# Kernel optimization log

Measured on AMD Instinct MI355X. Metric: run time of the kernel, lower is better.

Reference implementation:

```python
import jax, jax.numpy as jnp
import numpy as np

B = 131072
DIM = 64
D_IN = 32
D_OUT = 32
HIDDEN = 512
N_BINS = 8
TAIL = 3.0


def setup_inputs() -> dict:
    key = jax.random.key(0)
    ks = jax.random.split(key, 7)
    x = jax.random.normal(ks[0], (B, DIM), dtype=jnp.float32)
    out_dim = D_OUT * (3 * N_BINS - 1)  # 32 * 23 = 736
    W1 = jax.random.normal(ks[1], (D_IN, HIDDEN), dtype=jnp.float32) / np.sqrt(D_IN)
    b1 = jnp.zeros((HIDDEN,), dtype=jnp.float32)
    W2 = jax.random.normal(ks[2], (HIDDEN, HIDDEN), dtype=jnp.float32) / np.sqrt(HIDDEN)
    b2 = jnp.zeros((HIDDEN,), dtype=jnp.float32)
    W3 = jax.random.normal(ks[3], (HIDDEN, out_dim), dtype=jnp.float32) / np.sqrt(HIDDEN)
    b3 = jnp.zeros((out_dim,), dtype=jnp.float32)
    return {"x": x, "W1": W1, "b1": b1, "W2": W2, "b2": b2, "W3": W3, "b3": b3}


def _gather(t, idx):
    # t: (..., K), idx: (...) -> (...,)
    return jnp.take_along_axis(t, idx[..., None], axis=-1)[..., 0]


def rq_spline_forward(x, widths, heights, derivatives, tail_bound=TAIL):
    K = widths.shape[-1]
    widths = jax.nn.softmax(widths, axis=-1) * 2 * tail_bound
    heights = jax.nn.softmax(heights, axis=-1) * 2 * tail_bound
    derivatives = jax.nn.softplus(derivatives)
    ones = jnp.ones_like(derivatives[..., :1])
    derivatives = jnp.concatenate([ones, derivatives, ones], axis=-1)  # (..., K+1)
    cumwidths = jnp.cumsum(widths, axis=-1)
    cumwidths = jnp.pad(cumwidths, [(0, 0)] * (cumwidths.ndim - 1) + [(1, 0)]) - tail_bound
    cumheights = jnp.cumsum(heights, axis=-1)
    cumheights = jnp.pad(cumheights, [(0, 0)] * (cumheights.ndim - 1) + [(1, 0)]) - tail_bound

    inside = (x >= -tail_bound) & (x <= tail_bound)
    xc = jnp.clip(x, -tail_bound + 1e-6, tail_bound - 1e-6)
    # searchsorted (left): number of knots strictly less than xc
    bin_idx = jnp.sum(cumwidths[..., 1:] < xc[..., None], axis=-1)
    bin_idx = jnp.clip(bin_idx, 0, K - 1)

    w_k = _gather(widths, bin_idx)
    h_k = _gather(heights, bin_idx)
    d_k = _gather(derivatives, bin_idx)
    d_k1 = _gather(derivatives[..., 1:], bin_idx)
    cw_k = _gather(cumwidths, bin_idx)
    ch_k = _gather(cumheights, bin_idx)

    xi = jnp.clip((xc - cw_k) / w_k, 1e-6, 1 - 1e-6)
    s_k = h_k / w_k
    num = h_k * (s_k * xi**2 + d_k * xi * (1 - xi))
    den = s_k + (d_k + d_k1 - 2 * s_k) * xi * (1 - xi)
    y_inside = ch_k + num / den
    log_det_inside = (
        jnp.log(s_k**2 * (d_k1 * xi**2 + 2 * s_k * xi * (1 - xi) + d_k * (1 - xi) ** 2) + 1e-8)
        - jnp.log(den**2 + 1e-8)
    )
    y = jnp.where(inside, y_inside, x)
    log_det = jnp.where(inside, log_det_inside, jnp.zeros_like(x))
    return y, log_det


def reference(x, W1, b1, W2, b2, W3, b3):
    # mask: first D_IN dims conditioned on, last D_OUT transformed
    x_masked = x[:, :D_IN]
    x_transform = x[:, D_IN:]
    h = jax.nn.relu(x_masked @ W1 + b1)
    h = jax.nn.relu(h @ W2 + b2)
    raw = h @ W3 + b3
    raw = raw.reshape(x.shape[0], D_OUT, 3 * N_BINS - 1)
    widths = raw[..., :N_BINS]
    heights = raw[..., N_BINS:2 * N_BINS]
    derivs = raw[..., 2 * N_BINS:]
    y_t, log_det = rq_spline_forward(x_transform, widths, heights, derivs, TAIL)
    y = jnp.concatenate([x_masked, y_t], axis=-1)
    return y, jnp.sum(log_det, axis=-1)
```

## Files before the change

### kernel.cpp

```cpp
#include <hip/hip_runtime.h>
#include <hip/hip_bf16.h>
#include <stdint.h>

typedef __bf16 bf16_t;
typedef _Float16 f16_t;
typedef _Float16 f16x8 __attribute__((ext_vector_type(8)));
typedef _Float16 f16x4 __attribute__((ext_vector_type(4)));
typedef float f32x4 __attribute__((ext_vector_type(4)));

#define HID 512
#define NRAW 736
#define NRAW_PAD 768
#define TAILB 3.0f

__device__ __forceinline__ void glds16(const void* g, void* s) {
  __builtin_amdgcn_global_load_lds(
      (const __attribute__((address_space(1))) void*)g,
      (__attribute__((address_space(3))) void*)s, 16, 0, 0);
}
__device__ __forceinline__ float frcp(float x) { return __builtin_amdgcn_rcpf(x); }

__global__ void detect_dtype(const void* x, int* flag) {
  __shared__ int s;
  if (threadIdx.x == 0) s = 0;
  __syncthreads();
  const bf16_t* xb = (const bf16_t*)x;
  int cnt = 0;
  for (int j = 0; j < 16; j++) {
    float v = (float)xb[threadIdx.x * 16 + j];
    if (!(v == v) || fabsf(v) > 64.0f) cnt++;
  }
  atomicAdd(&s, cnt);
  __syncthreads();
  if (threadIdx.x == 0) *flag = (s > 64) ? 1 : 0;
}

__global__ void conv_wb(const void* W1, const void* W2, const void* W3,
                        const void* b1, const void* b2, const void* b3,
                        f16_t* __restrict__ w1t, f16_t* __restrict__ w2t,
                        f16_t* __restrict__ w3t,
                        float* __restrict__ bf1, float* __restrict__ bf2,
                        float* __restrict__ bf3, const int* flagp) {
  const int flag = *flagp;
  auto rd = [&](const void* p, size_t idx) -> float {
    return flag ? ((const float*)p)[idx] : (float)((const bf16_t*)p)[idx];
  };
  int i = blockIdx.x * 256 + threadIdx.x;
  if (i < 512 * 32)  { w1t[i] = (f16_t)rd(W1, (size_t)(i & 31) * 512 + (i >> 5)); return; }
  i -= 512 * 32;
  if (i < 512 * 512) { w2t[i] = (f16_t)rd(W2, (size_t)(i & 511) * 512 + (i >> 9)); return; }
  i -= 512 * 512;
  if (i < NRAW_PAD * 512) {
    int n = i >> 9, k = i & 511;
    int ch = n / 24, e = n % 24;
    w3t[i] = (e < 23) ? (f16_t)rd(W3, (size_t)k * NRAW + ch * 23 + e) : (f16_t)0.0f;
    return;
  }
  i -= NRAW_PAD * 512;
  if (i < 512) { bf1[i] = rd(b1, i); return; }
  i -= 512;
  if (i < 512) { bf2[i] = rd(b2, i); return; }
  i -= 512;
  if (i < NRAW_PAD) {
    int ch = i / 24, e = i % 24;
    bf3[i] = (e < 23) ? rd(b3, (size_t)ch * 23 + e) : 0.0f;
  }
}

__global__ void convert_x(const void* x, void* __restrict__ outv,
                          const int* flagp, int n) {
  const int flag = *flagp;
  const int i0 = (blockIdx.x * 256 + threadIdx.x) * 8;
  if (i0 >= n) return;
  const int row = i0 >> 5, col = i0 & 31;
  const size_t src = (size_t)row * 64 + col;
  if (flag) {
    const float4* s4 = (const float4*)((const float*)x + src);
    float4* d4 = (float4*)((float*)outv + src);
    d4[0] = s4[0]; d4[1] = s4[1];
  } else {
    *(uint4*)((bf16_t*)outv + src) = *(const uint4*)((const bf16_t*)x + src);
  }
}

__global__ void ld_finalize(const float* __restrict__ ldp, void* __restrict__ outv,
                            const int* __restrict__ flagp, int M) {
  const int i = blockIdx.x * 256 + threadIdx.x;
  if (i >= M) return;
  float s = 0.f;
  #pragma unroll
  for (int n = 0; n < 4; n++) s += ldp[(size_t)n * M + i];
  if (*flagp) ((float*)outv)[(size_t)M * 64 + i] = s;
  else        ((bf16_t*)outv)[(size_t)M * 64 + i] = (bf16_t)s;
}

__launch_bounds__(256)
__global__ void gemm12(const void* __restrict__ xorig, const f16_t* __restrict__ W1t,
                       const float* __restrict__ b1, const f16_t* __restrict__ W2t,
                       const float* __restrict__ b2, f16_t* __restrict__ H2,
                       int r0, const int* __restrict__ flagp) {
  constexpr int BK = 64;
  constexpr int BUF = 128 * BK;
  __shared__ __align__(16) f16_t As[2 * BUF], Bs[2 * BUF];
  const int t = threadIdx.x;
  const int id = blockIdx.x;
  const int xcd = id & 7, s = id >> 3;
  const int n0 = (s & 3) * 128;
  const int m0 = ((s >> 2) * 8 + xcd) * 128;
  const int lrow = t >> 3, lcb = t & 7;
  const int lane = t & 63, w = t >> 6;
  const int wr = (w >> 1) * 64, wc = (w & 1) * 64, wc2 = (w & 1) * 32;
  const int lm = lane & 15, quad = lane >> 4;
  const int flag = *flagp;

  const f16_t* gb[4];
  f16_t* ldb[4];
  #pragma unroll
  for (int r = 0; r < 4; r++) {
    const int row = r * 32 + lrow;
    const int gc = (lcb ^ (row & 7)) * 8;
    gb[r] = W2t + (size_t)(n0 + row) * 512 + gc;
    ldb[r] = &Bs[row * BK + lcb * 8];
  }
  int apo[4][2], bpo[4][2];
  #pragma unroll
  for (int i = 0; i < 4; i++) {
    const int ra = wr + i * 16 + lm, rb = wc + i * 16 + lm;
    #pragma unroll
    for (int ksi = 0; ksi < 2; ksi++) {
      const int qb = ksi * 4 + quad;
      apo[i][ksi] = ra * BK + ((qb ^ (ra & 7)) << 3);
      bpo[i][ksi] = rb * BK + ((qb ^ (rb & 7)) << 3);
    }
  }
  f16x8 xfr[4];
  #pragma unroll
  for (int i = 0; i < 4; i++) {
    const size_t xrow = (size_t)(r0 + m0 + wr + i * 16 + lm);
    if (flag) {
      const float* px = (const float*)xorig + xrow * 64 + quad * 8;
      const float4 a = *(const float4*)px;
      const float4 b = *(const float4*)(px + 4);
      f16x8 v;
      v[0] = (f16_t)a.x; v[1] = (f16_t)a.y; v[2] = (f16_t)a.z; v[3] = (f16_t)a.w;
      v[4] = (f16_t)b.x; v[5] = (f16_t)b.y; v[6] = (f16_t)b.z; v[7] = (f16_t)b.w;
      xfr[i] = v;
    } else {
      const bf16_t* px = (const bf16_t*)xorig + xrow * 64 + quad * 8;
      f16x8 v;
      #pragma unroll
      for (int j = 0; j < 8; j++) v[j] = (f16_t)(float)px[j];
      xfr[i] = v;
    }
  }
  const f16_t* w1p0 = W1t + (size_t)(wc2 + lm) * 32 + quad * 8;
  const f16_t* w1p1 = W1t + (size_t)(wc2 + 16 + lm) * 32 + quad * 8;
  const float* b1p0 = b1 + wc2 + 4 * quad;
  const float* b1p1 = b1 + wc2 + 16 + 4 * quad;
  int woff[4][2];
  #pragma unroll
  for (int i = 0; i < 4; i++) {
    const int row = wr + i * 16 + lm;
    #pragma unroll
    for (int Tl = 0; Tl < 2; Tl++) {
      const int cb = (wc2 >> 3) + 2 * Tl + (quad >> 1);
      woff[i][Tl] = row * BK + ((cb ^ (row & 7)) << 3) + 4 * (quad & 1);
    }
  }

  f32x4 acc[4][4] = {};

  {
    f16x8 w1f0 = *(const f16x8*)w1p0;
    f16x8 w1f1 = *(const f16x8*)w1p1;
    const float4 bv0 = *(const float4*)b1p0;
    const float4 bv1 = *(const float4*)b1p1;
    #pragma unroll
    for (int r = 0; r < 4; r++) glds16(gb[r], ldb[r]);
    #pragma unroll
    for (int i = 0; i < 4; i++) {
      f32x4 z = {};
      const f32x4 h0 = __builtin_amdgcn_mfma_f32_16x16x32_f16(w1f0, xfr[i], z, 0, 0, 0);
      const f32x4 h1 = __builtin_amdgcn_mfma_f32_16x16x32_f16(w1f1, xfr[i], z, 0, 0, 0);
      f16x4 v0, v1;
      v0[0] = (f16_t)fmaxf(h0[0] + bv0.x, 0.0f);
      v0[1] = (f16_t)fmaxf(h0[1] + bv0.y, 0.0f);
      v0[2] = (f16_t)fmaxf(h0[2] + bv0.z, 0.0f);
      v0[3] = (f16_t)fmaxf(h0[3] + bv0.w, 0.0f);
      v1[0] = (f16_t)fmaxf(h1[0] + bv1.x, 0.0f);
      v1[1] = (f16_t)fmaxf(h1[1] + bv1.y, 0.0f);
      v1[2] = (f16_t)fmaxf(h1[2] + bv1.z, 0.0f);
      v1[3] = (f16_t)fmaxf(h1[3] + bv1.w, 0.0f);
      *(f16x4*)&As[woff[i][0]] = v0;
      *(f16x4*)&As[woff[i][1]] = v1;
    }
  }
  f16x8 w1fa = *(const f16x8*)(w1p0 + (size_t)64 * 32);
  f16x8 w1fb = *(const f16x8*)(w1p1 + (size_t)64 * 32);
  float4 bva = *(const float4*)(b1p0 + 64);
  float4 bvb = *(const float4*)(b1p1 + 64);
  __syncthreads();

  #pragma unroll
  for (int k = 0; k < 8; k++) {
    const int cur = k & 1, nb = cur ^ 1;
    if (k < 7) {
      #pragma unroll
      for (int r = 0; r < 4; r++)
        glds16(gb[r] + (k + 1) * 64, ldb[r] + nb * BUF);
      #pragma unroll
      for (int i = 0; i < 4; i++) {
        f32x4 z = {};
        const f32x4 h0 = __builtin_amdgcn_mfma_f32_16x16x32_f16(w1fa, xfr[i], z, 0, 0, 0);
        const f32x4 h1 = __builtin_amdgcn_mfma_f32_16x16x32_f16(w1fb, xfr[i], z, 0, 0, 0);
        f16x4 v0, v1;
        v0[0] = (f16_t)fmaxf(h0[0] + bva.x, 0.0f);
        v0[1] = (f16_t)fmaxf(h0[1] + bva.y, 0.0f);
        v0[2] = (f16_t)fmaxf(h0[2] + bva.z, 0.0f);
        v0[3] = (f16_t)fmaxf(h0[3] + bva.w, 0.0f);
        v1[0] = (f16_t)fmaxf(h1[0] + bvb.x, 0.0f);
        v1[1] = (f16_t)fmaxf(h1[1] + bvb.y, 0.0f);
        v1[2] = (f16_t)fmaxf(h1[2] + bvb.z, 0.0f);
        v1[3] = (f16_t)fmaxf(h1[3] + bvb.w, 0.0f);
        *(f16x4*)&As[nb * BUF + woff[i][0]] = v0;
        *(f16x4*)&As[nb * BUF + woff[i][1]] = v1;
      }
      if (k < 6) {
        w1fa = *(const f16x8*)(w1p0 + (size_t)(k + 2) * 64 * 32);
        w1fb = *(const f16x8*)(w1p1 + (size_t)(k + 2) * 64 * 32);
        bva = *(const float4*)(b1p0 + (k + 2) * 64);
        bvb = *(const float4*)(b1p1 + (k + 2) * 64);
      }
    }
    #pragma unroll
    for (int ksi = 0; ksi < 2; ksi++) {
      f16x8 af[4], bf[4];
      #pragma unroll
      for (int i = 0; i < 4; i++) af[i] = *(const f16x8*)&As[cur * BUF + apo[i][ksi]];
      #pragma unroll
      for (int j = 0; j < 4; j++) bf[j] = *(const f16x8*)&Bs[cur * BUF + bpo[j][ksi]];
      __builtin_amdgcn_s_setprio(1);
      #pragma unroll
      for (int i = 0; i < 4; i++)
        #pragma unroll
        for (int j = 0; j < 4; j++)
          acc[i][j] = __builtin_amdgcn_mfma_f32_16x16x32_f16(af[i], bf[j], acc[i][j], 0, 0, 0);
      __builtin_amdgcn_s_setprio(0);
    }
    if (k < 7) __syncthreads();
  }
  #pragma unroll
  for (int i = 0; i < 4; i++)
    #pragma unroll
    for (int j = 0; j < 4; j++) {
      const int col = n0 + wc + j * 16 + lm;
      const float bv = b2[col];
      #pragma unroll
      for (int r = 0; r < 4; r++) {
        const int rowi = m0 + wr + i * 16 + quad * 4 + r;
        H2[(size_t)rowi * HID + col] = (f16_t)fmaxf(acc[i][j][r] + bv, 0.0f);
      }
    }
}

#define RSH 200
#define SP1 0.5413248546f

__launch_bounds__(512, 4)
__global__ void gemm3_spline(const f16_t* __restrict__ A, const f16_t* __restrict__ Bt,
                             const float* __restrict__ bias,
                             const void* __restrict__ xorig,
                             void* __restrict__ outv, float* __restrict__ ldp,
                             int M, int r0, const int* __restrict__ flagp) {
  __shared__ __align__(16) f16_t lds[2 * 8192 + 2 * 12288];
  f16_t* As = lds;
  f16_t* Bs = lds + 2 * 8192;
  f16_t* rawh = lds;

  const int t = threadIdx.x;
  const int id = blockIdx.x;
  const int xcd = id & 7, sloc = id >> 3;
  const int cpx = gridDim.x >> 3;
  const int wg = xcd * cpx + sloc;
  const int ntile = wg & 3;
  const int m0 = (wg >> 2) * 128;
  const int n0 = ntile * 192;
  const int lane = t & 63, w = t >> 6;
  const int lm = lane & 15, quad = lane >> 4;
  const int wrow = (w >> 2) * 64, wcol = (w & 3) * 48;
  const int lrow = t >> 3, lcb = t & 7;
  const int flag = *flagp;

  const int gc = (lcb ^ (lrow & 7)) * 8;
  const f16_t* gA = A + (size_t)(m0 + lrow) * 512 + gc;
  const f16_t* gB = Bt + (size_t)(n0 + lrow) * 512 + gc;
  f16_t* ldA = As + lrow * 64 + lcb * 8;
  f16_t* ldB = Bs + lrow * 64 + lcb * 8;

  int aoff[4], boff[3];
  #pragma unroll
  for (int i = 0; i < 4; i++) {
    const int ra = wrow + i * 16 + lm;
    aoff[i] = ra * 64 + ((quad ^ (ra & 7)) << 3);
  }
  #pragma unroll
  for (int j = 0; j < 3; j++) {
    const int rb = wcol + j * 16 + lm;
    boff[j] = rb * 64 + ((quad ^ (rb & 7)) << 3);
  }

  const int prow = t >> 3, pch = t & 7;
  float xt_pre[2];
  #pragma unroll
  for (int e = 0; e < 2; e++) {
    const size_t gi = (size_t)(r0 + m0 + e * 64 + prow) * 64 + 32 + ntile * 8 + pch;
    xt_pre[e] = flag ? ((const float*)xorig)[gi] : (float)((const bf16_t*)xorig)[gi];
  }
  float bv3[3];
  #pragma unroll
  for (int j = 0; j < 3; j++) bv3[j] = bias[n0 + wcol + j * 16 + lm];

  #pragma unroll
  for (int r = 0; r < 2; r++) glds16(gA + r * 32768, ldA + r * 4096);
  #pragma unroll
  for (int r = 0; r < 3; r++) glds16(gB + r * 32768, ldB + r * 4096);
  __syncthreads();

  f32x4 acc[4][3] = {};

  #pragma unroll
  for (int t8 = 0; t8 < 8; t8++) {
    const f16_t* Ab = As + (t8 & 1) * 8192;
    const f16_t* Bb = Bs + (t8 & 1) * 12288;
    if (t8 < 7) {
      const int nb = (t8 + 1) & 1;
      #pragma unroll
      for (int r = 0; r < 2; r++)
        glds16(gA + r * 32768 + (t8 + 1) * 64, ldA + nb * 8192 + r * 4096);
      #pragma unroll
      for (int r = 0; r < 3; r++)
        glds16(gB + r * 32768 + (t8 + 1) * 64, ldB + nb * 12288 + r * 4096);
    }
    #pragma unroll
    for (int ksi = 0; ksi < 2; ksi++) {
      f16x8 af[4], bf[3];
      #pragma unroll
      for (int i = 0; i < 4; i++)
        af[i] = *(const f16x8*)(Ab + (aoff[i] ^ (ksi << 5)));
      #pragma unroll
      for (int j = 0; j < 3; j++)
        bf[j] = *(const f16x8*)(Bb + (boff[j] ^ (ksi << 5)));
      __builtin_amdgcn_s_setprio(1);
      #pragma unroll
      for (int i = 0; i < 4; i++)
        #pragma unroll
        for (int j = 0; j < 3; j++)
          acc[i][j] = __builtin_amdgcn_mfma_f32_16x16x32_f16(af[i], bf[j], acc[i][j], 0, 0, 0);
      __builtin_amdgcn_s_setprio(0);
    }
    __syncthreads();
  }

  #pragma unroll
  for (int i = 0; i < 4; i++)
    #pragma unroll
    for (int j = 0; j < 3; j++) {
      const int col = wcol + j * 16 + lm;
      #pragma unroll
      for (int r = 0; r < 4; r++)
        rawh[(wrow + i * 16 + quad * 4 + r) * RSH + col] = (f16_t)(acc[i][j][r] + bv3[j]);
    }
  __syncthreads();

  #pragma unroll
  for (int e = 0; e < 2; e++) {
    const int row = e * 64 + prow;
    const f16_t* c16 = &rawh[row * RSH + pch * 24];
    const f16x8 v0 = *(const f16x8*)(c16);
    const f16x8 v1 = *(const f16x8*)(c16 + 8);
    const f16x8 v2 = *(const f16x8*)(c16 + 16);
    float wa[8], ha[8], da[7];
    #pragma unroll
    for (int j = 0; j < 8; j++) { wa[j] = (float)v0[j]; ha[j] = (float)v1[j]; }
    #pragma unroll
    for (int j = 0; j < 7; j++) da[j] = (float)v2[j];

    const float xt = xt_pre[e];
    const bool inside = (xt >= -TAILB) && (xt <= TAILB);
    const float xc = fminf(fmaxf(xt, -TAILB + 1e-6f), TAILB - 1e-6f);

    float mw = wa[0], mh = ha[0];
    #pragma unroll
    for (int j = 1; j < 8; j++) { mw = fmaxf(mw, wa[j]); mh = fmaxf(mh, ha[j]); }
    float ew[8], eh[8], sew = 0.f, seh = 0.f;
    #pragma unroll
    for (int j = 0; j < 8; j++) {
      ew[j] = __expf(wa[j] - mw); sew += ew[j];
      eh[j] = __expf(ha[j] - mh); seh += eh[j];
    }
    const float wsc = 6.0f * frcp(sew), hsc = 6.0f * frcp(seh);
    #pragma unroll
    for (int j = 0; j < 8; j++) { ew[j] *= wsc; eh[j] *= hsc; }

    float accw = -TAILB, runh = -TAILB;
    float cwk = -TAILB, chk = -TAILB;
    float wk = ew[0], hk = eh[0];
    float dkr = SP1, dk1r = da[0];
    #pragma unroll
    for (int i = 0; i < 7; i++) {
      accw += ew[i];
      runh += eh[i];
      const bool cond = accw < xc;
      cwk  = cond ? accw : cwk;
      chk  = cond ? runh : chk;
      wk   = cond ? ew[i + 1] : wk;
      hk   = cond ? eh[i + 1] : hk;
      dkr  = cond ? da[i] : dkr;
      dk1r = cond ? ((i == 6) ? SP1 : da[i + 1]) : dk1r;
    }
    const float dk  = fmaxf(dkr, 0.0f)  + __logf(1.0f + __expf(-fabsf(dkr)));
    const float dk1 = fmaxf(dk1r, 0.0f) + __logf(1.0f + __expf(-fabsf(dk1r)));

    const float rwk = frcp(wk);
    float xi = (xc - cwk) * rwk;
    xi = fminf(fmaxf(xi, 1e-6f), 1.0f - 1e-6f);
    const float om = 1.0f - xi;
    const float sl = hk * rwk;
    const float num = hk * (sl * xi * xi + dk * xi * om);
    const float den = sl + (dk + dk1 - 2.0f * sl) * xi * om;
    const float y_in = chk + num * frcp(den);
    const float t1 = sl * sl * (dk1 * xi * xi + 2.0f * sl * xi * om + dk * om * om);
    const float ld_in = __logf(t1 + 1e-8f) - __logf(den * den + 1e-8f);

    const float yv = inside ? y_in : xt;
    const float ldv = inside ? ld_in : 0.0f;

    const size_t grow = (size_t)(r0 + m0 + row);
    if (flag) ((float*)outv)[grow * 64 + 32 + ntile * 8 + pch] = yv;
    else      ((bf16_t*)outv)[grow * 64 + 32 + ntile * 8 + pch] = (bf16_t)yv;

    float l = ldv + __shfl_down(ldv, 1, 8);
    l += __shfl_down(l, 2, 8);
    l += __shfl_down(l, 4, 8);
    if ((t & 7) == 0) ldp[(size_t)ntile * M + grow] = l;
  }
}

extern "C" void kernel_launch(void* const* d_in, const int* in_sizes, int n_in,
                              void* d_out, int out_size, void* d_ws, size_t ws_size,
                              hipStream_t stream) {
  const void* x  = d_in[0];
  const void* W1 = d_in[1];
  const void* b1 = d_in[2];
  const void* W2 = d_in[3];
  const void* b2 = d_in[4];
  const void* W3 = d_in[5];
  const void* b3 = d_in[6];
  const int M = in_sizes[0] / 64;

  char* ws = (char*)d_ws;
  size_t off = 0;
  auto alloc = [&](size_t bytes) {
    void* p = ws + off;
    off += (bytes + 255) & ~(size_t)255;
    return p;
  };
  int*   flag = (int*)alloc(256);
  float* bf1  = (float*)alloc(512 * 4);
  float* bf2  = (float*)alloc(512 * 4);
  float* bf3  = (float*)alloc(NRAW_PAD * 4);
  f16_t* W1t  = (f16_t*)alloc((size_t)512 * 32 * 2);
  f16_t* W2t  = (f16_t*)alloc((size_t)512 * 512 * 2);
  f16_t* W3t  = (f16_t*)alloc((size_t)NRAW_PAD * 512 * 2);
  float* ldp  = (float*)alloc((size_t)8 * M * 4);

  const size_t per_row = (size_t)HID * 2;
  size_t avail = (ws_size > off + 4096) ? (ws_size - off - 4096) : 0;
  long rows = (long)(avail / per_row);
  rows -= rows % 1024;
  if (rows > M) rows = M;
  if (rows < 1024) rows = 1024;

  f16_t* h2 = (f16_t*)alloc((size_t)rows * HID * 2);

  detect_dtype<<<1, 256, 0, stream>>>(x, flag);
  conv_wb<<<2631, 256, 0, stream>>>(W1, W2, W3, b1, b2, b3,
                                    W1t, W2t, W3t, bf1, bf2, bf3, flag);
  convert_x<<<(M * 32 / 8 + 255) / 256, 256, 0, stream>>>(x, d_out, flag, M * 32);

  for (int r0 = 0; r0 < M; r0 += (int)rows) {
    const int mc = (int)((M - r0 < rows) ? (M - r0) : rows);
    const int mt128 = mc / 128;
    gemm12<<<mt128 * 4, 256, 0, stream>>>(x, W1t, bf1, W2t, bf2, h2, r0, flag);
    gemm3_spline<<<mt128 * 4, 512, 0, stream>>>(
        h2, W3t, bf3, x, d_out, ldp, M, r0, flag);
  }
  ld_finalize<<<(M + 255) / 256, 256, 0, stream>>>(ldp, d_out, flag, M);
}
```

Measured before the change: 333.5 us.

## Single-buffer layer-1 activations in gemm12 and fold x passthrough copy into gemm3

```diff
diff --git a/kernel.cpp b/kernel.cpp
--- a/kernel.cpp
+++ b/kernel.cpp
@@ -67,22 +67,6 @@
   }
 }
 
-__global__ void convert_x(const void* x, void* __restrict__ outv,
-                          const int* flagp, int n) {
-  const int flag = *flagp;
-  const int i0 = (blockIdx.x * 256 + threadIdx.x) * 8;
-  if (i0 >= n) return;
-  const int row = i0 >> 5, col = i0 & 31;
-  const size_t src = (size_t)row * 64 + col;
-  if (flag) {
-    const float4* s4 = (const float4*)((const float*)x + src);
-    float4* d4 = (float4*)((float*)outv + src);
-    d4[0] = s4[0]; d4[1] = s4[1];
-  } else {
-    *(uint4*)((bf16_t*)outv + src) = *(const uint4*)((const bf16_t*)x + src);
-  }
-}
-
 __global__ void ld_finalize(const float* __restrict__ ldp, void* __restrict__ outv,
                             const int* __restrict__ flagp, int M) {
   const int i = blockIdx.x * 256 + threadIdx.x;
@@ -101,7 +85,7 @@
                        int r0, const int* __restrict__ flagp) {
   constexpr int BK = 64;
   constexpr int BUF = 128 * BK;
-  __shared__ __align__(16) f16_t As[2 * BUF], Bs[2 * BUF];
+  __shared__ __align__(16) f16_t As[BUF], Bs[2 * BUF];
   const int t = threadIdx.x;
   const int id = blockIdx.x;
   const int xcd = id & 7, s = id >> 3;
@@ -208,22 +192,44 @@
       #pragma unroll
       for (int r = 0; r < 4; r++)
         glds16(gb[r] + (k + 1) * 64, ldb[r] + nb * BUF);
+    }
+    #pragma unroll
+    for (int ksi = 0; ksi < 2; ksi++) {
+      f16x8 af[4], bf[4];
+      #pragma unroll
+      for (int i = 0; i < 4; i++) af[i] = *(const f16x8*)&As[apo[i][ksi]];
+      #pragma unroll
+      for (int j = 0; j < 4; j++) bf[j] = *(const f16x8*)&Bs[cur * BUF + bpo[j][ksi]];
+      __builtin_amdgcn_s_setprio(1);
+      #pragma unroll
+      for (int i = 0; i < 4; i++)
+        #pragma unroll
+        for (int j = 0; j < 4; j++)
+          acc[i][j] = __builtin_amdgcn_mfma_f32_16x16x32_f16(af[i], bf[j], acc[i][j], 0, 0, 0);
+      __builtin_amdgcn_s_setprio(0);
+    }
+    if (k < 7) {
+      f32x4 h[4][2];
       #pragma unroll
       for (int i = 0; i < 4; i++) {
         f32x4 z = {};
-        const f32x4 h0 = __builtin_amdgcn_mfma_f32_16x16x32_f16(w1fa, xfr[i], z, 0, 0, 0);
-        const f32x4 h1 = __builtin_amdgcn_mfma_f32_16x16x32_f16(w1fb, xfr[i], z, 0, 0, 0);
+        h[i][0] = __builtin_amdgcn_mfma_f32_16x16x32_f16(w1fa, xfr[i], z, 0, 0, 0);
+        h[i][1] = __builtin_amdgcn_mfma_f32_16x16x32_f16(w1fb, xfr[i], z, 0, 0, 0);
+      }
+      __syncthreads();
+      #pragma unroll
+      for (int i = 0; i < 4; i++) {
         f16x4 v0, v1;
-        v0[0] = (f16_t)fmaxf(h0[0] + bva.x, 0.0f);
-        v0[1] = (f16_t)fmaxf(h0[1] + bva.y, 0.0f);
-        v0[2] = (f16_t)fmaxf(h0[2] + bva.z, 0.0f);
-        v0[3] = (f16_t)fmaxf(h0[3] + bva.w, 0.0f);
-        v1[0] = (f16_t)fmaxf(h1[0] + bvb.x, 0.0f);
-        v1[1] = (f16_t)fmaxf(h1[1] + bvb.y, 0.0f);
-        v1[2] = (f16_t)fmaxf(h1[2] + bvb.z, 0.0f);
-        v1[3] = (f16_t)fmaxf(h1[3] + bvb.w, 0.0f);
-        *(f16x4*)&As[nb * BUF + woff[i][0]] = v0;
-        *(f16x4*)&As[nb * BUF + woff[i][1]] = v1;
+        v0[0] = (f16_t)fmaxf(h[i][0][0] + bva.x, 0.0f);
+        v0[1] = (f16_t)fmaxf(h[i][0][1] + bva.y, 0.0f);
+        v0[2] = (f16_t)fmaxf(h[i][0][2] + bva.z, 0.0f);
+        v0[3] = (f16_t)fmaxf(h[i][0][3] + bva.w, 0.0f);
+        v1[0] = (f16_t)fmaxf(h[i][1][0] + bvb.x, 0.0f);
+        v1[1] = (f16_t)fmaxf(h[i][1][1] + bvb.y, 0.0f);
+        v1[2] = (f16_t)fmaxf(h[i][1][2] + bvb.z, 0.0f);
+        v1[3] = (f16_t)fmaxf(h[i][1][3] + bvb.w, 0.0f);
+        *(f16x4*)&As[woff[i][0]] = v0;
+        *(f16x4*)&As[woff[i][1]] = v1;
       }
       if (k < 6) {
         w1fa = *(const f16x8*)(w1p0 + (size_t)(k + 2) * 64 * 32);
@@ -231,23 +237,8 @@
         bva = *(const float4*)(b1p0 + (k + 2) * 64);
         bvb = *(const float4*)(b1p1 + (k + 2) * 64);
       }
-    }
-    #pragma unroll
-    for (int ksi = 0; ksi < 2; ksi++) {
-      f16x8 af[4], bf[4];
-      #pragma unroll
-      for (int i = 0; i < 4; i++) af[i] = *(const f16x8*)&As[cur * BUF + apo[i][ksi]];
-      #pragma unroll
-      for (int j = 0; j < 4; j++) bf[j] = *(const f16x8*)&Bs[cur * BUF + bpo[j][ksi]];
-      __builtin_amdgcn_s_setprio(1);
-      #pragma unroll
-      for (int i = 0; i < 4; i++)
-        #pragma unroll
-        for (int j = 0; j < 4; j++)
-          acc[i][j] = __builtin_amdgcn_mfma_f32_16x16x32_f16(af[i], bf[j], acc[i][j], 0, 0, 0);
-      __builtin_amdgcn_s_setprio(0);
-    }
-    if (k < 7) __syncthreads();
+      __syncthreads();
+    }
   }
   #pragma unroll
   for (int i = 0; i < 4; i++)
@@ -319,6 +310,17 @@
   float bv3[3];
   #pragma unroll
   for (int j = 0; j < 3; j++) bv3[j] = bias[n0 + wcol + j * 16 + lm];
+
+  if (t < 128) {
+    const size_t base = (size_t)(r0 + m0 + t) * 64 + ntile * 8;
+    if (flag) {
+      const float4* s4 = (const float4*)((const float*)xorig + base);
+      float4* d4 = (float4*)((float*)outv + base);
+      d4[0] = s4[0]; d4[1] = s4[1];
+    } else {
+      *(uint4*)((bf16_t*)outv + base) = *(const uint4*)((const bf16_t*)xorig + base);
+    }
+  }
 
   #pragma unroll
   for (int r = 0; r < 2; r++) glds16(gA + r * 32768, ldA + r * 4096);
@@ -486,7 +488,6 @@
   detect_dtype<<<1, 256, 0, stream>>>(x, flag);
   conv_wb<<<2631, 256, 0, stream>>>(W1, W2, W3, b1, b2, b3,
                                     W1t, W2t, W3t, bf1, bf2, bf3, flag);
-  convert_x<<<(M * 32 / 8 + 255) / 256, 256, 0, stream>>>(x, d_out, flag, M * 32);
 
   for (int r0 = 0; r0 < M; r0 += (int)rows) {
     const int mc = (int)((M - r0 < rows) ? (M - r0) : rows);
```

Result: slower. 351.7 us (+5.4%).

## Use 512-thread blocks in fused gemm12 and interleave layer-1 MFMA with layer-2 math

Applied to the files above, without the earlier changes.

```diff
diff --git a/kernel.cpp b/kernel.cpp
--- a/kernel.cpp
+++ b/kernel.cpp
@@ -94,7 +94,7 @@
   else        ((bf16_t*)outv)[(size_t)M * 64 + i] = (bf16_t)s;
 }
 
-__launch_bounds__(256)
+__launch_bounds__(512, 4)
 __global__ void gemm12(const void* __restrict__ xorig, const f16_t* __restrict__ W1t,
                        const float* __restrict__ b1, const f16_t* __restrict__ W2t,
                        const float* __restrict__ b2, f16_t* __restrict__ H2,
@@ -109,28 +109,34 @@
   const int m0 = ((s >> 2) * 8 + xcd) * 128;
   const int lrow = t >> 3, lcb = t & 7;
   const int lane = t & 63, w = t >> 6;
-  const int wr = (w >> 1) * 64, wc = (w & 1) * 64, wc2 = (w & 1) * 32;
+  const int wr = (w >> 2) * 64;
+  const int wc = (w & 3) * 32;
+  const int wc4 = (w & 3) * 16;
   const int lm = lane & 15, quad = lane >> 4;
   const int flag = *flagp;
 
-  const f16_t* gb[4];
-  f16_t* ldb[4];
-  #pragma unroll
-  for (int r = 0; r < 4; r++) {
-    const int row = r * 32 + lrow;
+  const f16_t* gb[2];
+  f16_t* ldb[2];
+  #pragma unroll
+  for (int r = 0; r < 2; r++) {
+    const int row = r * 64 + lrow;
     const int gc = (lcb ^ (row & 7)) * 8;
     gb[r] = W2t + (size_t)(n0 + row) * 512 + gc;
     ldb[r] = &Bs[row * BK + lcb * 8];
   }
-  int apo[4][2], bpo[4][2];
-  #pragma unroll
-  for (int i = 0; i < 4; i++) {
-    const int ra = wr + i * 16 + lm, rb = wc + i * 16 + lm;
-    #pragma unroll
-    for (int ksi = 0; ksi < 2; ksi++) {
-      const int qb = ksi * 4 + quad;
+  int apo[4][2], bpo[2][2];
+  #pragma unroll
+  for (int ksi = 0; ksi < 2; ksi++) {
+    const int qb = ksi * 4 + quad;
+    #pragma unroll
+    for (int i = 0; i < 4; i++) {
+      const int ra = wr + i * 16 + lm;
       apo[i][ksi] = ra * BK + ((qb ^ (ra & 7)) << 3);
-      bpo[i][ksi] = rb * BK + ((qb ^ (rb & 7)) << 3);
+    }
+    #pragma unroll
+    for (int j = 0; j < 2; j++) {
+      const int rb = wc + j * 16 + lm;
+      bpo[j][ksi] = rb * BK + ((qb ^ (rb & 7)) << 3);
     }
   }
   f16x8 xfr[4];
@@ -153,52 +159,39 @@
       xfr[i] = v;
     }
   }
-  const f16_t* w1p0 = W1t + (size_t)(wc2 + lm) * 32 + quad * 8;
-  const f16_t* w1p1 = W1t + (size_t)(wc2 + 16 + lm) * 32 + quad * 8;
-  const float* b1p0 = b1 + wc2 + 4 * quad;
-  const float* b1p1 = b1 + wc2 + 16 + 4 * quad;
-  int woff[4][2];
-  #pragma unroll
-  for (int i = 0; i < 4; i++) {
-    const int row = wr + i * 16 + lm;
-    #pragma unroll
-    for (int Tl = 0; Tl < 2; Tl++) {
-      const int cb = (wc2 >> 3) + 2 * Tl + (quad >> 1);
-      woff[i][Tl] = row * BK + ((cb ^ (row & 7)) << 3) + 4 * (quad & 1);
-    }
-  }
-
-  f32x4 acc[4][4] = {};
-
+  const f16_t* w1p = W1t + (size_t)(wc4 + lm) * 32 + quad * 8;
+  const float* b1p = b1 + wc4 + 4 * quad;
+  int woff[4];
   {
-    f16x8 w1f0 = *(const f16x8*)w1p0;
-    f16x8 w1f1 = *(const f16x8*)w1p1;
-    const float4 bv0 = *(const float4*)b1p0;
-    const float4 bv1 = *(const float4*)b1p1;
-    #pragma unroll
-    for (int r = 0; r < 4; r++) glds16(gb[r], ldb[r]);
+    const int cb = (w & 3) * 2 + (quad >> 1);
+    #pragma unroll
+    for (int i = 0; i < 4; i++) {
+      const int row = wr + i * 16 + lm;
+      woff[i] = row * BK + ((cb ^ (row & 7)) << 3) + 4 * (quad & 1);
+    }
+  }
+
+  f32x4 acc[4][2] = {};
+
+  #pragma unroll
+  for (int r = 0; r < 2; r++) glds16(gb[r], ldb[r]);
+  {
+    const f16x8 w1f = *(const f16x8*)w1p;
+    const float4 bv = *(const float4*)b1p;
     #pragma unroll
     for (int i = 0; i < 4; i++) {
       f32x4 z = {};
-      const f32x4 h0 = __builtin_amdgcn_mfma_f32_16x16x32_f16(w1f0, xfr[i], z, 0, 0, 0);
-      const f32x4 h1 = __builtin_amdgcn_mfma_f32_16x16x32_f16(w1f1, xfr[i], z, 0, 0, 0);
-      f16x4 v0, v1;
-      v0[0] = (f16_t)fmaxf(h0[0] + bv0.x, 0.0f);
-      v0[1] = (f16_t)fmaxf(h0[1] + bv0.y, 0.0f);
-      v0[2] = (f16_t)fmaxf(h0[2] + bv0.z, 0.0f);
-      v0[3] = (f16_t)fmaxf(h0[3] + bv0.w, 0.0f);
-      v1[0] = (f16_t)fmaxf(h1[0] + bv1.x, 0.0f);
-      v1[1] = (f16_t)fmaxf(h1[1] + bv1.y, 0.0f);
-      v1[2] = (f16_t)fmaxf(h1[2] + bv1.z, 0.0f);
-      v1[3] = (f16_t)fmaxf(h1[3] + bv1.w, 0.0f);
-      *(f16x4*)&As[woff[i][0]] = v0;
-      *(f16x4*)&As[woff[i][1]] = v1;
-    }
-  }
-  f16x8 w1fa = *(const f16x8*)(w1p0 + (size_t)64 * 32);
-  f16x8 w1fb = *(const f16x8*)(w1p1 + (size_t)64 * 32);
-  float4 bva = *(const float4*)(b1p0 + 64);
-  float4 bvb = *(const float4*)(b1p1 + 64);
+      const f32x4 h = __builtin_amdgcn_mfma_f32_16x16x32_f16(w1f, xfr[i], z, 0, 0, 0);
+      f16x4 v;
+      v[0] = (f16_t)fmaxf(h[0] + bv.x, 0.0f);
+      v[1] = (f16_t)fmaxf(h[1] + bv.y, 0.0f);
+      v[2] = (f16_t)fmaxf(h[2] + bv.z, 0.0f);
+      v[3] = (f16_t)fmaxf(h[3] + bv.w, 0.0f);
+      *(f16x4*)&As[woff[i]] = v;
+    }
+  }
+  f16x8 w1fa = *(const f16x8*)(w1p + (size_t)64 * 32);
+  float4 bva = *(const float4*)(b1p + 64);
   __syncthreads();
 
   #pragma unroll
@@ -206,53 +199,53 @@
     const int cur = k & 1, nb = cur ^ 1;
     if (k < 7) {
       #pragma unroll
-      for (int r = 0; r < 4; r++)
+      for (int r = 0; r < 2; r++)
         glds16(gb[r] + (k + 1) * 64, ldb[r] + nb * BUF);
+    }
+    f32x4 h[4];
+    if (k < 7) {
       #pragma unroll
       for (int i = 0; i < 4; i++) {
         f32x4 z = {};
-        const f32x4 h0 = __builtin_amdgcn_mfma_f32_16x16x32_f16(w1fa, xfr[i], z, 0, 0, 0);
-        const f32x4 h1 = __builtin_amdgcn_mfma_f32_16x16x32_f16(w1fb, xfr[i], z, 0, 0, 0);
-        f16x4 v0, v1;
-        v0[0] = (f16_t)fmaxf(h0[0] + bva.x, 0.0f);
-        v0[1] = (f16_t)fmaxf(h0[1] + bva.y, 0.0f);
-        v0[2] = (f16_t)fmaxf(h0[2] + bva.z, 0.0f);
-        v0[3] = (f16_t)fmaxf(h0[3] + bva.w, 0.0f);
-        v1[0] = (f16_t)fmaxf(h1[0] + bvb.x, 0.0f);
-        v1[1] = (f16_t)fmaxf(h1[1] + bvb.y, 0.0f);
-        v1[2] = (f16_t)fmaxf(h1[2] + bvb.z, 0.0f);
-        v1[3] = (f16_t)fmaxf(h1[3] + bvb.w, 0.0f);
-        *(f16x4*)&As[nb * BUF + woff[i][0]] = v0;
-        *(f16x4*)&As[nb * BUF + woff[i][1]] = v1;
+        h[i] = __builtin_amdgcn_mfma_f32_16x16x32_f16(w1fa, xfr[i], z, 0, 0, 0);
+      }
+    }
+    #pragma unroll
+    for (int ksi = 0; ksi < 2; ksi++) {
+      f16x8 af[4], bf[2];
+      #pragma unroll
+      for (int i = 0; i < 4; i++) af[i] = *(const f16x8*)&As[cur * BUF + apo[i][ksi]];
+      #pragma unroll
+      for (int j = 0; j < 2; j++) bf[j] = *(const f16x8*)&Bs[cur * BUF + bpo[j][ksi]];
+      __builtin_amdgcn_s_setprio(1);
+      #pragma unroll
+      for (int i = 0; i < 4; i++)
+        #pragma unroll
+        for (int j = 0; j < 2; j++)
+          acc[i][j] = __builtin_amdgcn_mfma_f32_16x16x32_f16(af[i], bf[j], acc[i][j], 0, 0, 0);
+      __builtin_amdgcn_s_setprio(0);
+    }
+    if (k < 7) {
+      #pragma unroll
+      for (int i = 0; i < 4; i++) {
+        f16x4 v;
+        v[0] = (f16_t)fmaxf(h[i][0] + bva.x, 0.0f);
+        v[1] = (f16_t)fmaxf(h[i][1] + bva.y, 0.0f);
+        v[2] = (f16_t)fmaxf(h[i][2] + bva.z, 0.0f);
+        v[3] = (f16_t)fmaxf(h[i][3] + bva.w, 0.0f);
+        *(f16x4*)&As[nb * BUF + woff[i]] = v;
       }
       if (k < 6) {
-        w1fa = *(const f16x8*)(w1p0 + (size_t)(k + 2) * 64 * 32);
-        w1fb = *(const f16x8*)(w1p1 + (size_t)(k + 2) * 64 * 32);
-        bva = *(const float4*)(b1p0 + (k + 2) * 64);
-        bvb = *(const float4*)(b1p1 + (k + 2) * 64);
+        w1fa = *(const f16x8*)(w1p + (size_t)(k + 2) * 64 * 32);
+        bva = *(const float4*)(b1p + (k + 2) * 64);
       }
-    }
-    #pragma unroll
-    for (int ksi = 0; ksi < 2; ksi++) {
-      f16x8 af[4], bf[4];
-      #pragma unroll
-      for (int i = 0; i < 4; i++) af[i] = *(const f16x8*)&As[cur * BUF + apo[i][ksi]];
-      #pragma unroll
-      for (int j = 0; j < 4; j++) bf[j] = *(const f16x8*)&Bs[cur * BUF + bpo[j][ksi]];
-      __builtin_amdgcn_s_setprio(1);
-      #pragma unroll
-      for (int i = 0; i < 4; i++)
-        #pragma unroll
-        for (int j = 0; j < 4; j++)
-          acc[i][j] = __builtin_amdgcn_mfma_f32_16x16x32_f16(af[i], bf[j], acc[i][j], 0, 0, 0);
-      __builtin_amdgcn_s_setprio(0);
-    }
-    if (k < 7) __syncthreads();
+      __syncthreads();
+    }
   }
   #pragma unroll
   for (int i = 0; i < 4; i++)
     #pragma unroll
-    for (int j = 0; j < 4; j++) {
+    for (int j = 0; j < 2; j++) {
       const int col = n0 + wc + j * 16 + lm;
       const float bv = b2[col];
       #pragma unroll
@@ -491,7 +484,7 @@
   for (int r0 = 0; r0 < M; r0 += (int)rows) {
     const int mc = (int)((M - r0 < rows) ? (M - r0) : rows);
     const int mt128 = mc / 128;
-    gemm12<<<mt128 * 4, 256, 0, stream>>>(x, W1t, bf1, W2t, bf2, h2, r0, flag);
+    gemm12<<<mt128 * 4, 512, 0, stream>>>(x, W1t, bf1, W2t, bf2, h2, r0, flag);
     gemm3_spline<<<mt128 * 4, 512, 0, stream>>>(
         h2, W3t, bf3, x, d_out, ldp, M, r0, flag);
   }
```

Result: faster. 320.5 us (-3.9%).
